# Kernel tuning notes

Measured on AMD Instinct MI355X. Metric: run time of the kernel, lower is better.

Reference implementation:

```python
import jax, jax.numpy as jnp
import numpy as np

N_NODES = 50000
N_EDGES = 800000
D_IN = 64
D_OUT = 64
D_U = 64


def setup_inputs() -> dict:
    key = jax.random.key(0)
    ks = jax.random.split(key, 6)
    x = jax.random.normal(ks[0], (N_NODES, D_IN), dtype=jnp.float32)
    edge_index = jax.random.randint(ks[1], (2, N_EDGES), 0, N_NODES, dtype=jnp.int64)
    edge_weight = jax.random.uniform(ks[2], (N_EDGES,), dtype=jnp.float32)
    u = jax.random.normal(ks[3], (N_NODES, D_U), dtype=jnp.float32)
    # xavier-uniform-like init for W and A
    limW = float(np.sqrt(6.0 / (D_IN + D_OUT)))
    W = jax.random.uniform(ks[4], (D_IN, D_OUT), minval=-limW, maxval=limW, dtype=jnp.float32)
    limA = float(np.sqrt(6.0 / (D_U + D_OUT)))
    A = jax.random.uniform(ks[5], (D_U, D_OUT), minval=-limA, maxval=limA, dtype=jnp.float32)
    bias = jnp.zeros((D_OUT,), dtype=jnp.float32)
    return {"x": x, "edge_index": edge_index, "edge_weight": edge_weight,
            "u": u, "W": W, "A": A, "bias": bias}


def reference(x, edge_index, edge_weight, u, W, A, bias):
    # Non-negative weights via softplus (input-convex constraint)
    W_nn = jax.nn.softplus(W)                      # [D_in, D_out]
    # Transform all nodes once, then gather per edge (equivalent to x[src] @ W per edge)
    h = x @ W_nn                                   # [N, D_out]
    src, dst = edge_index[0], edge_index[1]
    msgs = h[src] * edge_weight[:, None]           # [E, D_out]
    out = jax.ops.segment_sum(msgs, dst, num_segments=x.shape[0])  # [N, D_out]
    out = out + u @ jax.nn.softplus(A) + bias
    return jax.nn.relu(out)
```

## Files before the change

### kernel.cpp

```cpp
#include <hip/hip_runtime.h>

#define NN 50000
#define NE 800000
#define DD 64
#define CAP 64
#define XPAD 68
#define NBT 782
#define NBS 3125

__global__ __launch_bounds__(256, 4) void k_fused(
    const float* __restrict__ x, const float* __restrict__ u,
    const float* __restrict__ W, const float* __restrict__ A,
    const float* __restrict__ bias,
    const int* __restrict__ ei, const float* __restrict__ ew,
    int* __restrict__ cursor, float2* __restrict__ slots,
    float* __restrict__ h, float* __restrict__ base) {
    __shared__ float sW[DD * DD];
    __shared__ float sx[64 * XPAD];

    const int tid = threadIdx.x;
    int b = blockIdx.x;

    if (b < NBS) {
        int e = b * 256 + tid;
        if (e < NE) {
            int s = ei[e];
            int d = ei[NE + e];
            float w = ew[e];
            int pos = atomicAdd(&cursor[d], 1);
            if (pos < CAP) {
                float2 v;
                v.x = __int_as_float(s);
                v.y = w;
                slots[(size_t)d * CAP + pos] = v;
            }
        }
        return;
    }
    b -= NBS;
    const int phase = (b >= NBT) ? 1 : 0;
    const int bx = phase ? b - NBT : b;
    const float* __restrict__ in = phase ? u : x;
    const float* __restrict__ wm = phase ? A : W;
    float* __restrict__ op = phase ? base : h;
    const int r0 = bx * 64;
    const int nrow = min(64, NN - r0);
    const int tr = tid >> 4;
    const int tc = tid & 15;

    {
        const float4* w4 = (const float4*)wm;
        #pragma unroll
        for (int i = tid; i < DD * DD / 4; i += 256) {
            float4 v = w4[i];
            v.x = fmaxf(v.x, 0.f) + log1pf(expf(-fabsf(v.x)));
            v.y = fmaxf(v.y, 0.f) + log1pf(expf(-fabsf(v.y)));
            v.z = fmaxf(v.z, 0.f) + log1pf(expf(-fabsf(v.z)));
            v.w = fmaxf(v.w, 0.f) + log1pf(expf(-fabsf(v.w)));
            *(float4*)&sW[i * 4] = v;
        }
    }
    {
        const float4* x4 = (const float4*)(in + (size_t)r0 * DD);
        const int n4 = nrow * (DD / 4);
        #pragma unroll
        for (int i = tid; i < 64 * (DD / 4); i += 256) {
            float4 v = (i < n4) ? x4[i] : make_float4(0.f, 0.f, 0.f, 0.f);
            *(float4*)&sx[(i >> 4) * XPAD + (i & 15) * 4] = v;
        }
    }
    __syncthreads();

    float4 bv = make_float4(0.f, 0.f, 0.f, 0.f);
    if (phase) bv = *(const float4*)&bias[tc * 4];
    float4 acc[4] = {bv, bv, bv, bv};

    #pragma unroll 4
    for (int k4 = 0; k4 < DD / 4; ++k4) {
        float4 w0 = *(const float4*)&sW[(k4 * 4 + 0) * DD + tc * 4];
        float4 w1 = *(const float4*)&sW[(k4 * 4 + 1) * DD + tc * 4];
        float4 w2 = *(const float4*)&sW[(k4 * 4 + 2) * DD + tc * 4];
        float4 w3 = *(const float4*)&sW[(k4 * 4 + 3) * DD + tc * 4];
        #pragma unroll
        for (int i = 0; i < 4; ++i) {
            float4 xv = *(const float4*)&sx[(tr * 4 + i) * XPAD + k4 * 4];
            acc[i].x += xv.x * w0.x + xv.y * w1.x + xv.z * w2.x + xv.w * w3.x;
            acc[i].y += xv.x * w0.y + xv.y * w1.y + xv.z * w2.y + xv.w * w3.y;
            acc[i].z += xv.x * w0.z + xv.y * w1.z + xv.z * w2.z + xv.w * w3.z;
            acc[i].w += xv.x * w0.w + xv.y * w1.w + xv.z * w2.w + xv.w * w3.w;
        }
    }
    #pragma unroll
    for (int i = 0; i < 4; ++i) {
        int r = r0 + tr * 4 + i;
        if (r < NN) *(float4*)&op[(size_t)r * DD + tc * 4] = acc[i];
    }
}

__global__ __launch_bounds__(256, 8) void k_apply(
    const int* __restrict__ cursor, const float2* __restrict__ slots,
    const float* __restrict__ h, float* __restrict__ out) {
    int wid = (blockIdx.x * 256 + threadIdx.x) >> 6;
    int lane = threadIdx.x & 63;
    if (wid >= NN) return;
    int deg = min(cursor[wid], CAP);
    const float2* sl = slots + (size_t)wid * CAP;
    float acc = 0.f;
    int i = 0;
    for (; i + 4 <= deg; i += 4) {
        float4 p0 = *(const float4*)(sl + i);
        float4 p1 = *(const float4*)(sl + i + 2);
        int s0 = __float_as_int(p0.x), s1 = __float_as_int(p0.z);
        int s2 = __float_as_int(p1.x), s3 = __float_as_int(p1.z);
        float h0 = h[(size_t)s0 * DD + lane];
        float h1 = h[(size_t)s1 * DD + lane];
        float h2 = h[(size_t)s2 * DD + lane];
        float h3 = h[(size_t)s3 * DD + lane];
        acc += h0 * p0.y + h1 * p0.w + h2 * p1.y + h3 * p1.w;
    }
    for (; i < deg; ++i) {
        float2 v = sl[i];
        acc += h[(size_t)__float_as_int(v.x) * DD + lane] * v.y;
    }
    size_t o = (size_t)wid * DD + lane;
    out[o] = fmaxf(out[o] + acc, 0.f);
}

extern "C" void kernel_launch(void* const* d_in, const int* in_sizes, int n_in,
                              void* d_out, int out_size, void* d_ws, size_t ws_size,
                              hipStream_t stream) {
    const float* x    = (const float*)d_in[0];
    const int*   ei   = (const int*)d_in[1];
    const float* ew   = (const float*)d_in[2];
    const float* u    = (const float*)d_in[3];
    const float* W    = (const float*)d_in[4];
    const float* A    = (const float*)d_in[5];
    const float* bias = (const float*)d_in[6];
    float* out = (float*)d_out;
    float* ws  = (float*)d_ws;

    float*  h      = ws;
    int*    cursor = (int*)(ws + NN * DD);
    float2* slots  = (float2*)(ws + NN * DD + NN);

    hipMemsetAsync(cursor, 0, NN * sizeof(int), stream);
    k_fused<<<NBS + 2 * NBT, 256, 0, stream>>>(x, u, W, A, bias, ei, ew,
                                               cursor, slots, h, out);
    k_apply<<<(NN * 64 + 255) / 256, 256, 0, stream>>>(cursor, slots, h, out);
}
```

Before: 203.2 us.

## Split fused kernel, transpose slot layout, fold u@softplus(A) into apply

Splits the fused scatter-plus-transform kernel into separate scatter and transform kernels. The edge slot buffer changes from node-major to slot-major, so the scatter writes and the apply reads are laid out differently. The u@softplus(A)+bias term is now computed inside the apply kernel from a shared-memory copy of softplus(A), which removes one N×64 write and read of the output base. The cost is an extra kernel launch, a softplus(A) recomputation in every apply block, and per-lane redundant reads of u rows that are broadcast across the wave.

```diff
diff --git a/kernel.cpp b/kernel.cpp
--- a/kernel.cpp
+++ b/kernel.cpp
@@ -5,51 +5,38 @@
 #define DD 64
 #define CAP 64
 #define XPAD 68
-#define NBT 782
-#define NBS 3125
 
-__global__ __launch_bounds__(256, 4) void k_fused(
-    const float* __restrict__ x, const float* __restrict__ u,
-    const float* __restrict__ W, const float* __restrict__ A,
-    const float* __restrict__ bias,
+__global__ __launch_bounds__(256) void k_scatter(
     const int* __restrict__ ei, const float* __restrict__ ew,
-    int* __restrict__ cursor, float2* __restrict__ slots,
-    float* __restrict__ h, float* __restrict__ base) {
+    int* __restrict__ cursor, float2* __restrict__ slots) {
+    int e = blockIdx.x * 256 + threadIdx.x;
+    if (e >= NE) return;
+    int s = ei[e];
+    int d = ei[NE + e];
+    float w = ew[e];
+    int pos = atomicAdd(&cursor[d], 1);
+    if (pos < CAP) {
+        float2 v;
+        v.x = __int_as_float(s);
+        v.y = w;
+        slots[(size_t)pos * NN + d] = v;
+    }
+}
+
+__global__ __launch_bounds__(256, 4) void k_transform(
+    const float* __restrict__ x, const float* __restrict__ W,
+    float* __restrict__ h) {
     __shared__ float sW[DD * DD];
     __shared__ float sx[64 * XPAD];
 
     const int tid = threadIdx.x;
-    int b = blockIdx.x;
-
-    if (b < NBS) {
-        int e = b * 256 + tid;
-        if (e < NE) {
-            int s = ei[e];
-            int d = ei[NE + e];
-            float w = ew[e];
-            int pos = atomicAdd(&cursor[d], 1);
-            if (pos < CAP) {
-                float2 v;
-                v.x = __int_as_float(s);
-                v.y = w;
-                slots[(size_t)d * CAP + pos] = v;
-            }
-        }
-        return;
-    }
-    b -= NBS;
-    const int phase = (b >= NBT) ? 1 : 0;
-    const int bx = phase ? b - NBT : b;
-    const float* __restrict__ in = phase ? u : x;
-    const float* __restrict__ wm = phase ? A : W;
-    float* __restrict__ op = phase ? base : h;
-    const int r0 = bx * 64;
-    const int nrow = min(64, NN - r0);
     const int tr = tid >> 4;
     const int tc = tid & 15;
+    const int r0 = blockIdx.x * 64;
+    const int nrow = min(64, NN - r0);
 
     {
-        const float4* w4 = (const float4*)wm;
+        const float4* w4 = (const float4*)W;
         #pragma unroll
         for (int i = tid; i < DD * DD / 4; i += 256) {
             float4 v = w4[i];
@@ -61,7 +48,7 @@
         }
     }
     {
-        const float4* x4 = (const float4*)(in + (size_t)r0 * DD);
+        const float4* x4 = (const float4*)(x + (size_t)r0 * DD);
         const int n4 = nrow * (DD / 4);
         #pragma unroll
         for (int i = tid; i < 64 * (DD / 4); i += 256) {
@@ -71,10 +58,7 @@
     }
     __syncthreads();
 
-    float4 bv = make_float4(0.f, 0.f, 0.f, 0.f);
-    if (phase) bv = *(const float4*)&bias[tc * 4];
-    float4 acc[4] = {bv, bv, bv, bv};
-
+    float4 acc[4] = {{0,0,0,0},{0,0,0,0},{0,0,0,0},{0,0,0,0}};
     #pragma unroll 4
     for (int k4 = 0; k4 < DD / 4; ++k4) {
         float4 w0 = *(const float4*)&sW[(k4 * 4 + 0) * DD + tc * 4];
@@ -93,37 +77,67 @@
     #pragma unroll
     for (int i = 0; i < 4; ++i) {
         int r = r0 + tr * 4 + i;
-        if (r < NN) *(float4*)&op[(size_t)r * DD + tc * 4] = acc[i];
+        if (r < NN) *(float4*)&h[(size_t)r * DD + tc * 4] = acc[i];
     }
 }
 
 __global__ __launch_bounds__(256, 8) void k_apply(
     const int* __restrict__ cursor, const float2* __restrict__ slots,
-    const float* __restrict__ h, float* __restrict__ out) {
-    int wid = (blockIdx.x * 256 + threadIdx.x) >> 6;
-    int lane = threadIdx.x & 63;
-    if (wid >= NN) return;
-    int deg = min(cursor[wid], CAP);
-    const float2* sl = slots + (size_t)wid * CAP;
+    const float* __restrict__ h, const float* __restrict__ u,
+    const float* __restrict__ A, const float* __restrict__ bias,
+    float* __restrict__ out) {
+    __shared__ float sA[DD * DD];
+
+    const int tid = threadIdx.x;
+    {
+        const float4* a4 = (const float4*)A;
+        #pragma unroll
+        for (int i = tid; i < DD * DD / 4; i += 256) {
+            float4 v = a4[i];
+            v.x = fmaxf(v.x, 0.f) + log1pf(expf(-fabsf(v.x)));
+            v.y = fmaxf(v.y, 0.f) + log1pf(expf(-fabsf(v.y)));
+            v.z = fmaxf(v.z, 0.f) + log1pf(expf(-fabsf(v.z)));
+            v.w = fmaxf(v.w, 0.f) + log1pf(expf(-fabsf(v.w)));
+            *(float4*)&sA[i * 4] = v;
+        }
+    }
+    __syncthreads();
+
+    const int wid = (blockIdx.x * 256 + tid) >> 6;
+    const int lane = tid & 63;
+
+    float base = bias[lane];
+    {
+        const float4* u4 = (const float4*)(u + (size_t)wid * DD);
+        #pragma unroll 4
+        for (int k4 = 0; k4 < DD / 4; ++k4) {
+            float4 uv = u4[k4];
+            base += uv.x * sA[(k4 * 4 + 0) * DD + lane]
+                  + uv.y * sA[(k4 * 4 + 1) * DD + lane]
+                  + uv.z * sA[(k4 * 4 + 2) * DD + lane]
+                  + uv.w * sA[(k4 * 4 + 3) * DD + lane];
+        }
+    }
+
+    const int deg = min(cursor[wid], CAP);
     float acc = 0.f;
     int i = 0;
     for (; i + 4 <= deg; i += 4) {
-        float4 p0 = *(const float4*)(sl + i);
-        float4 p1 = *(const float4*)(sl + i + 2);
-        int s0 = __float_as_int(p0.x), s1 = __float_as_int(p0.z);
-        int s2 = __float_as_int(p1.x), s3 = __float_as_int(p1.z);
-        float h0 = h[(size_t)s0 * DD + lane];
-        float h1 = h[(size_t)s1 * DD + lane];
-        float h2 = h[(size_t)s2 * DD + lane];
-        float h3 = h[(size_t)s3 * DD + lane];
-        acc += h0 * p0.y + h1 * p0.w + h2 * p1.y + h3 * p1.w;
+        float2 e0 = slots[(size_t)(i + 0) * NN + wid];
+        float2 e1 = slots[(size_t)(i + 1) * NN + wid];
+        float2 e2 = slots[(size_t)(i + 2) * NN + wid];
+        float2 e3 = slots[(size_t)(i + 3) * NN + wid];
+        float h0 = h[(size_t)__float_as_int(e0.x) * DD + lane];
+        float h1 = h[(size_t)__float_as_int(e1.x) * DD + lane];
+        float h2 = h[(size_t)__float_as_int(e2.x) * DD + lane];
+        float h3 = h[(size_t)__float_as_int(e3.x) * DD + lane];
+        acc += h0 * e0.y + h1 * e1.y + h2 * e2.y + h3 * e3.y;
     }
     for (; i < deg; ++i) {
-        float2 v = sl[i];
-        acc += h[(size_t)__float_as_int(v.x) * DD + lane] * v.y;
+        float2 ev = slots[(size_t)i * NN + wid];
+        acc += h[(size_t)__float_as_int(ev.x) * DD + lane] * ev.y;
     }
-    size_t o = (size_t)wid * DD + lane;
-    out[o] = fmaxf(out[o] + acc, 0.f);
+    out[(size_t)wid * DD + lane] = fmaxf(base + acc, 0.f);
 }
 
 extern "C" void kernel_launch(void* const* d_in, const int* in_sizes, int n_in,
@@ -144,7 +158,7 @@
     float2* slots  = (float2*)(ws + NN * DD + NN);
 
     hipMemsetAsync(cursor, 0, NN * sizeof(int), stream);
-    k_fused<<<NBS + 2 * NBT, 256, 0, stream>>>(x, u, W, A, bias, ei, ew,
-                                               cursor, slots, h, out);
-    k_apply<<<(NN * 64 + 255) / 256, 256, 0, stream>>>(cursor, slots, h, out);
+    k_scatter<<<(NE + 255) / 256, 256, 0, stream>>>(ei, ew, cursor, slots);
+    k_transform<<<(NN + 63) / 64, 256, 0, stream>>>(x, W, h);
+    k_apply<<<NN / 4, 256, 0, stream>>>(cursor, slots, h, u, A, bias, out);
 }
```

Result: slower. 299.1 us (+47.2%).
